# Performance work log

Measured on AMD Instinct MI355X. Metric: run time of the kernel, lower is better.

## Reference

```python
import jax, jax.numpy as jnp
import numpy as np

# ---- config (CSA layer, layer_idx=0 of pattern 'CSA,HCA') ----
B, T, C = 2, 2048, 2048
NH, NKV = 16, 8
HD = C // NH            # 128 head dim
ROPE_DIM = HD // 2      # partial RoPE dims (rope_head_dim=0 default)
RATIO = 4               # csa_compress_ratio
G = T // RATIO          # compressed groups (T divisible by ratio -> no pad)
IDX_NH = NH
IDX_HD = max(8, C // NH // 2)  # 64
TOPK = 64               # index_topk
Q_RANK = C // 2         # _default_rank
O_RPG = C // 2          # o_proj rank_per_group, o_groups=1


def rms_norm(x, eps=1e-6):
    return x * jax.lax.rsqrt(jnp.mean(jnp.square(x), axis=-1, keepdims=True) + eps)


def _rope(x, cos, sin):
    d = x.shape[-1] // 2
    x1, x2 = x[..., :d], x[..., d:]
    return jnp.concatenate([x1 * cos + x2 * sin, -x1 * sin + x2 * cos], axis=-1)


def partial_rope(x, cos, sin):
    # rotate only the last ROPE_DIM dims; cos/sin: [..., ROPE_DIM//2]
    xn, xr = x[..., :-ROPE_DIM], x[..., -ROPE_DIM:]
    return jnp.concatenate([xn, _rope(xr, cos, sin)], axis=-1)


def setup_inputs() -> dict:
    key = jax.random.key(0)
    ks = jax.random.split(key, 16)
    s = 0.02
    x = jax.random.normal(ks[0], (B, T, C), jnp.float32)
    pos = jnp.arange(T, dtype=jnp.float32)
    inv = 10000.0 ** (-jnp.arange(0, HD // 2, dtype=jnp.float32) / (HD // 2))
    ang = pos[:, None] * inv[None, :]  # [T, HD//2]
    p = lambda i, shp: jax.random.normal(ks[i], shp, jnp.float32) * s
    return dict(
        x=x, cos=jnp.cos(ang), sin=jnp.sin(ang),
        q_a_w=p(1, (C, Q_RANK)), q_b_w=p(2, (Q_RANK, NH * HD)),
        ck_w=p(3, (C, NKV * HD)), cv_w=p(4, (C, NKV * HD)), cg_w=p(5, (C, NKV * HD)),
        c_ape=p(6, (RATIO, NKV, HD)),
        iq_w=p(7, (C, IDX_NH * IDX_HD)), ik_w=p(8, (C, IDX_NH * IDX_HD)),
        ig_w=p(9, (C, IDX_NH * IDX_HD)), i_ape=p(10, (RATIO, IDX_NH, IDX_HD)),
        sink=jnp.zeros((NH,), jnp.float32),
        o_wa=p(11, (1, O_RPG, C)), o_pb=p(12, (O_RPG, C)),
    )


def reference(x, cos, sin, q_a_w, q_b_w, ck_w, cv_w, cg_w, c_ape,
              iq_w, ik_w, ig_w, i_ape, sink, o_wa, o_pb):
    NEG = jnp.finfo(jnp.float32).min
    half = ROPE_DIM // 2
    # --- low-rank queries + partial RoPE ---
    q = (x @ q_a_w @ q_b_w).reshape(B, T, NH, HD)
    q = partial_rope(q, cos[None, :, None, :half], sin[None, :, None, :half])
    # --- GatedCompressor: learned gated pooling over blocks of RATIO ---
    k = (x @ ck_w).reshape(B, G, RATIO, NKV, HD)
    v = (x @ cv_w).reshape(B, G, RATIO, NKV, HD)
    g = (x @ cg_w).reshape(B, G, RATIO, NKV, HD) + c_ape[None, None]
    w = jax.nn.softmax(g, axis=2)
    ck = (k * w).sum(2)  # [B,G,NKV,HD]
    cv = (v * w).sum(2)
    group_ends = jnp.arange(RATIO - 1, T, RATIO)  # [G]
    ckr = partial_rope(ck, cos[group_ends][None, :, None, :half],
                       sin[group_ends][None, :, None, :half])
    # --- LightningIndexer: compressed indexer keys + per-token top-k groups ---
    ik = (x @ ik_w).reshape(B, G, RATIO, IDX_NH, IDX_HD)
    ig = (x @ ig_w).reshape(B, G, RATIO, IDX_NH, IDX_HD) + i_ape[None, None]
    iw = jax.nn.softmax(ig, axis=2)
    ikeys = rms_norm((ik * iw).sum(2))  # [B,G,IH,IHD]
    iq = rms_norm((x @ iq_w).reshape(B, T, IDX_NH, IDX_HD))
    iscore = jnp.einsum('bthd,bghd->bhtg', iq, ikeys) * IDX_HD ** -0.5
    iscore = iscore.mean(axis=1)  # [B,T,G]
    causal = group_ends[None, None, :] <= jnp.arange(T)[None, :, None]
    iscore = jnp.where(causal, iscore, NEG)
    sel = jax.lax.top_k(iscore, TOPK)[1]  # [B,T,K]
    bidx = jnp.arange(B)[:, None, None]
    tidx = jnp.arange(T)[None, :, None]
    mask = jnp.zeros((B, T, G), bool).at[bidx, tidx, sel].set(True) & causal
    # --- compressed sparse attention with sink, GQA expand ---
    rep = NH // NKV
    kk = jnp.repeat(ckr, rep, axis=2)  # [B,G,NH,HD]
    vv = jnp.repeat(cv, rep, axis=2)
    scores = jnp.einsum('bthd,bghd->bhtg', q, kk) * HD ** -0.5
    scores = jnp.where(mask[:, None], scores, NEG)
    sinkb = jnp.broadcast_to(sink.reshape(1, NH, 1, 1), (B, NH, T, 1))
    probs = jax.nn.softmax(jnp.concatenate([scores, sinkb], axis=-1), axis=-1)[..., :-1]
    out = jnp.einsum('bhtg,bghd->bthd', probs, vv).reshape(B, T, C)
    # --- GroupedOutputProjection (o_groups=1) ---
    h = jnp.einsum('btgd,grd->btgr', out.reshape(B, T, 1, C), o_wa).reshape(B, T, -1)
    return rms_norm(h) @ o_pb
```

## Files before the change

### kernel.cpp

```cpp
#include <hip/hip_runtime.h>
#include <hip/hip_bf16.h>
#include <math.h>

constexpr int Bn  = 2;
constexpr int Tn  = 2048;
constexpr int NHn = 16;
constexpr int NKVn= 8;
constexpr int Gn  = 512;
constexpr int TKn = 64;

typedef __attribute__((ext_vector_type(8))) __bf16 bf16x8;
typedef __attribute__((ext_vector_type(4))) __bf16 bf16x4;
typedef __attribute__((ext_vector_type(2))) __bf16 bf16x2;
typedef __attribute__((ext_vector_type(4))) float f32x4;

__device__ __forceinline__ void gload_lds16(const void* g, void* l) {
  __builtin_amdgcn_global_load_lds(
      (const __attribute__((address_space(1))) unsigned int*)g,
      (__attribute__((address_space(3))) unsigned int*)l, 16, 0, 0);
}

__global__ __launch_bounds__(512) void gemm_kvqa_8ph(
    const __bf16* __restrict__ A, const __bf16* __restrict__ Bt,
    float* __restrict__ Cf, __bf16* __restrict__ Cq)
{
  constexpr int K = 2048;
  constexpr int NT = K / 64;
  __shared__ __bf16 lds[2][2][2][256][32];
  const int tid = threadIdx.x;
  const int wid = tid >> 6, lane = tid & 63;
  const int wm = wid >> 2, wn = wid & 3;
  const int row0 = blockIdx.y * 256, col0 = blockIdx.x * 256;

  f32x4 acc[8][4];
  const f32x4 zero = {0.f, 0.f, 0.f, 0.f};
  #pragma unroll
  for (int i = 0; i < 8; ++i)
    #pragma unroll
    for (int j = 0; j < 4; ++j) acc[i][j] = zero;

  auto stage1 = [&](int kt, int op, int ph, int buf) {
    long k0 = (long)kt * 64 + ph * 32;
    const __bf16* src = op ? Bt : A;
    const int base0 = op ? col0 : row0;
    #pragma unroll
    for (int l = 0; l < 2; ++l) {
      int u = l * 512 + tid;
      int r = u >> 2, c4 = u & 3;
      long csrc = (long)((c4 ^ ((r >> 1) & 3)) * 8);
      gload_lds16(src + (long)(base0 + r) * K + k0 + csrc, &lds[buf][op][ph][r][c4 * 8]);
    }
  };

  stage1(0, 0, 0, 0);
  stage1(0, 1, 0, 0);
  stage1(0, 0, 1, 0);
  stage1(0, 1, 1, 0);
  asm volatile("s_waitcnt vmcnt(4)" ::: "memory");
  asm volatile("s_barrier" ::: "memory");

  for (int kt = 0; kt < NT; ++kt) {
    const int buf = kt & 1;
    const bool pre = (kt + 1 < NT);
    bf16x8 afA[4], afB[4], bf[4];

    #pragma unroll
    for (int i = 0; i < 4; ++i) {
      int r = wm * 128 + i * 16 + (lane & 15);
      int c4 = (lane >> 4) ^ ((r >> 1) & 3);
      afA[i] = *(const bf16x8*)&lds[buf][0][0][r][c4 * 8];
    }
    #pragma unroll
    for (int i = 0; i < 4; ++i) {
      int r = wn * 64 + i * 16 + (lane & 15);
      int c4 = (lane >> 4) ^ ((r >> 1) & 3);
      bf[i] = *(const bf16x8*)&lds[buf][1][0][r][c4 * 8];
    }
    if (pre) stage1(kt + 1, 0, 0, buf ^ 1);
    asm volatile("s_barrier" ::: "memory");
    asm volatile("s_waitcnt lgkmcnt(0)" ::: "memory");
    __builtin_amdgcn_sched_barrier(0);
    __builtin_amdgcn_s_setprio(1);
    #pragma unroll
    for (int i = 0; i < 4; ++i)
      #pragma unroll
      for (int j = 0; j < 4; ++j)
        acc[i][j] = __builtin_amdgcn_mfma_f32_16x16x32_bf16(afA[i], bf[j], acc[i][j], 0, 0, 0);
    __builtin_amdgcn_s_setprio(0);
    asm volatile("s_barrier" ::: "memory");

    #pragma unroll
    for (int i = 0; i < 4; ++i) {
      int r = wm * 128 + (i + 4) * 16 + (lane & 15);
      int c4 = (lane >> 4) ^ ((r >> 1) & 3);
      afB[i] = *(const bf16x8*)&lds[buf][0][0][r][c4 * 8];
    }
    if (pre) {
      stage1(kt + 1, 1, 0, buf ^ 1);
      asm volatile("s_waitcnt vmcnt(4)" ::: "memory");
    } else {
      asm volatile("s_waitcnt vmcnt(0)" ::: "memory");
    }
    asm volatile("s_barrier" ::: "memory");
    asm volatile("s_waitcnt lgkmcnt(0)" ::: "memory");
    __builtin_amdgcn_sched_barrier(0);
    __builtin_amdgcn_s_setprio(1);
    #pragma unroll
    for (int i = 0; i < 4; ++i)
      #pragma unroll
      for (int j = 0; j < 4; ++j)
        acc[i + 4][j] = __builtin_amdgcn_mfma_f32_16x16x32_bf16(afB[i], bf[j], acc[i + 4][j], 0, 0, 0);
    __builtin_amdgcn_s_setprio(0);
    asm volatile("s_barrier" ::: "memory");

    #pragma unroll
    for (int i = 0; i < 4; ++i) {
      int r = wm * 128 + i * 16 + (lane & 15);
      int c4 = (lane >> 4) ^ ((r >> 1) & 3);
      afA[i] = *(const bf16x8*)&lds[buf][0][1][r][c4 * 8];
    }
    #pragma unroll
    for (int i = 0; i < 4; ++i) {
      int r = wn * 64 + i * 16 + (lane & 15);
      int c4 = (lane >> 4) ^ ((r >> 1) & 3);
      bf[i] = *(const bf16x8*)&lds[buf][1][1][r][c4 * 8];
    }
    if (pre) stage1(kt + 1, 0, 1, buf ^ 1);
    asm volatile("s_barrier" ::: "memory");
    asm volatile("s_waitcnt lgkmcnt(0)" ::: "memory");
    __builtin_amdgcn_sched_barrier(0);
    __builtin_amdgcn_s_setprio(1);
    #pragma unroll
    for (int i = 0; i < 4; ++i)
      #pragma unroll
      for (int j = 0; j < 4; ++j)
        acc[i][j] = __builtin_amdgcn_mfma_f32_16x16x32_bf16(afA[i], bf[j], acc[i][j], 0, 0, 0);
    __builtin_amdgcn_s_setprio(0);
    asm volatile("s_barrier" ::: "memory");

    #pragma unroll
    for (int i = 0; i < 4; ++i) {
      int r = wm * 128 + (i + 4) * 16 + (lane & 15);
      int c4 = (lane >> 4) ^ ((r >> 1) & 3);
      afB[i] = *(const bf16x8*)&lds[buf][0][1][r][c4 * 8];
    }
    if (pre) {
      stage1(kt + 1, 1, 1, buf ^ 1);
      asm volatile("s_waitcnt vmcnt(4)" ::: "memory");
    }
    asm volatile("s_barrier" ::: "memory");
    asm volatile("s_waitcnt lgkmcnt(0)" ::: "memory");
    __builtin_amdgcn_sched_barrier(0);
    __builtin_amdgcn_s_setprio(1);
    #pragma unroll
    for (int i = 0; i < 4; ++i)
      #pragma unroll
      for (int j = 0; j < 4; ++j)
        acc[i + 4][j] = __builtin_amdgcn_mfma_f32_16x16x32_bf16(afB[i], bf[j], acc[i + 4][j], 0, 0, 0);
    __builtin_amdgcn_s_setprio(0);
    asm volatile("s_barrier" ::: "memory");
  }

  const int crow = (lane >> 4) * 4, ccol = lane & 15;
  const bool isQ = (col0 >= 3072);
  #pragma unroll
  for (int mf = 0; mf < 8; ++mf)
    #pragma unroll
    for (int nf = 0; nf < 4; ++nf)
      #pragma unroll
      for (int j = 0; j < 4; ++j) {
        long r = row0 + wm * 128 + mf * 16 + crow + j;
        long c = col0 + wn * 64 + nf * 16 + ccol;
        float v = acc[mf][nf][j];
        if (isQ) Cq[r * 1024 + (c - 3072)] = (__bf16)v;
        else     Cf[r * 3072 + c] = v;
      }
}

template<int EPI>
__global__ __launch_bounds__(256) void gemm_pipe(
    const __bf16* __restrict__ A, const __bf16* __restrict__ Bt,
    void* __restrict__ Cp, int N, int K,
    const float* __restrict__ cosb, const float* __restrict__ sinb,
    const float* __restrict__ rs)
{
  const int NT = K >> 6;
  __shared__ __bf16 lds[2][2][2][128][32];
  const int tid = threadIdx.x;
  const int wid = tid >> 6, lane = tid & 63;
  const int wm = wid >> 1, wn = wid & 1;
  const int row0 = blockIdx.y * 128, col0 = blockIdx.x * 128;

  f32x4 acc[4][4];
  const f32x4 zero = {0.f, 0.f, 0.f, 0.f};
  #pragma unroll
  for (int i = 0; i < 4; ++i)
    #pragma unroll
    for (int j = 0; j < 4; ++j) acc[i][j] = zero;

  auto stage = [&](int kt, int p, int buf) {
    long k0 = (long)kt * 64 + p * 32;
    #pragma unroll
    for (int l = 0; l < 2; ++l) {
      int u = l * 256 + tid;
      int r = u >> 2, c4 = u & 3;
      long csrc = (long)((c4 ^ ((r >> 1) & 3)) * 8);
      gload_lds16(A  + (long)(row0 + r) * K + k0 + csrc, &lds[buf][0][p][r][c4 * 8]);
      gload_lds16(Bt + (long)(col0 + r) * K + k0 + csrc, &lds[buf][1][p][r][c4 * 8]);
    }
  };

  stage(0, 0, 0);
  stage(0, 1, 0);

  for (int kt = 0; kt < NT; ++kt) {
    const int buf = kt & 1;
    #pragma unroll
    for (int ph = 0; ph < 2; ++ph) {
      if (kt + 1 < NT) {
        stage(kt + 1, ph, buf ^ 1);
        asm volatile("s_waitcnt vmcnt(8)" ::: "memory");
      } else {
        if (ph == 0) asm volatile("s_waitcnt vmcnt(4)" ::: "memory");
        else         asm volatile("s_waitcnt vmcnt(0)" ::: "memory");
      }
      asm volatile("s_barrier" ::: "memory");
      bf16x8 af[4], bfr[4];
      #pragma unroll
      for (int mf = 0; mf < 4; ++mf) {
        int r = wm * 64 + mf * 16 + (lane & 15);
        int c4 = (lane >> 4) ^ ((r >> 1) & 3);
        af[mf] = *(const bf16x8*)&lds[buf][0][ph][r][c4 * 8];
      }
      #pragma unroll
      for (int nf = 0; nf < 4; ++nf) {
        int r = wn * 64 + nf * 16 + (lane & 15);
        int c4 = (lane >> 4) ^ ((r >> 1) & 3);
        bfr[nf] = *(const bf16x8*)&lds[buf][1][ph][r][c4 * 8];
      }
      __builtin_amdgcn_s_setprio(1);
      #pragma unroll
      for (int mf = 0; mf < 4; ++mf)
        #pragma unroll
        for (int nf = 0; nf < 4; ++nf)
          acc[mf][nf] = __builtin_amdgcn_mfma_f32_16x16x32_bf16(af[mf], bfr[nf], acc[mf][nf], 0, 0, 0);
      __builtin_amdgcn_s_setprio(0);
      asm volatile("s_barrier" ::: "memory");
    }
  }

  const int crow = (lane >> 4) * 4, ccol = lane & 15;
  if constexpr (EPI == 1) {
    __bf16* C = (__bf16*)Cp;
    if (wn == 1) {
      #pragma unroll
      for (int mf = 0; mf < 4; ++mf)
        #pragma unroll
        for (int j = 0; j < 4; ++j) {
          long r = row0 + wm * 64 + mf * 16 + crow + j;
          int t = (int)(r & 2047);
          #pragma unroll
          for (int nfp = 0; nfp < 2; ++nfp) {
            int jj = nfp * 16 + ccol;
            float c = cosb[t * 64 + jj], s = sinb[t * 64 + jj];
            float x1 = acc[mf][nfp][j];
            float x2 = acc[mf][nfp + 2][j];
            C[r * N + col0 + 64 + jj] = (__bf16)(x1 * c + x2 * s);
            C[r * N + col0 + 96 + jj] = (__bf16)(-x1 * s + x2 * c);
          }
        }
    } else {
      #pragma unroll
      for (int mf = 0; mf < 4; ++mf)
        #pragma unroll
        for (int nf = 0; nf < 4; ++nf)
          #pragma unroll
          for (int j = 0; j < 4; ++j) {
            long r = row0 + wm * 64 + mf * 16 + crow + j;
            long c = col0 + nf * 16 + ccol;
            C[r * N + c] = (__bf16)acc[mf][nf][j];
          }
    }
  } else {
    #pragma unroll
    for (int mf = 0; mf < 4; ++mf)
      #pragma unroll
      for (int nf = 0; nf < 4; ++nf)
        #pragma unroll
        for (int j = 0; j < 4; ++j) {
          long r = row0 + wm * 64 + mf * 16 + crow + j;
          long c = col0 + wn * 64 + nf * 16 + ccol;
          float v = acc[mf][nf][j];
          if constexpr (EPI == 2)
            ((float*)Cp)[r * N + c] = v * rs[r];
          else
            ((__bf16*)Cp)[r * N + c] = (__bf16)v;
        }
  }
}

__global__ __launch_bounds__(256) void gemm_split(
    const __bf16* __restrict__ Ah, const __bf16* __restrict__ Al,
    const __bf16* __restrict__ Bh, const __bf16* __restrict__ Bl,
    float* __restrict__ C, int M, int N, int K, float alpha,
    long sA, long sB, long sC)
{
  const int NT = K >> 5;
  __shared__ __bf16 lds[2][4][128][32];
  const int tid = threadIdx.x;
  const int wid = tid >> 6, lane = tid & 63;
  const int wm = wid >> 1, wn = wid & 1;
  const int row0 = blockIdx.y * 128, col0 = blockIdx.x * 128;
  Ah += (long)blockIdx.z * sA;  Al += (long)blockIdx.z * sA;
  Bh += (long)blockIdx.z * sB;  Bl += (long)blockIdx.z * sB;

  f32x4 acc[4][4];
  const f32x4 zero = {0.f, 0.f, 0.f, 0.f};
  #pragma unroll
  for (int i = 0; i < 4; ++i)
    #pragma unroll
    for (int j = 0; j < 4; ++j) acc[i][j] = zero;

  auto stage = [&](int kt, int buf) {
    long k0 = (long)kt * 32;
    #pragma unroll
    for (int l = 0; l < 2; ++l) {
      int u = l * 256 + tid;
      int r = u >> 2, c4 = u & 3;
      long csrc = (long)((c4 ^ ((r >> 1) & 3)) * 8);
      long ga = (long)(row0 + r) * K + k0 + csrc;
      long gb = (long)(col0 + r) * K + k0 + csrc;
      gload_lds16(Ah + ga, &lds[buf][0][r][c4 * 8]);
      gload_lds16(Al + ga, &lds[buf][1][r][c4 * 8]);
      gload_lds16(Bh + gb, &lds[buf][2][r][c4 * 8]);
      gload_lds16(Bl + gb, &lds[buf][3][r][c4 * 8]);
    }
  };

  stage(0, 0);

  for (int kt = 0; kt < NT; ++kt) {
    const int buf = kt & 1;
    if (kt + 1 < NT) {
      stage(kt + 1, buf ^ 1);
      asm volatile("s_waitcnt vmcnt(8)" ::: "memory");
    } else {
      asm volatile("s_waitcnt vmcnt(0)" ::: "memory");
    }
    asm volatile("s_barrier" ::: "memory");
    bf16x8 ah[4], al[4], bh[4], bl[4];
    #pragma unroll
    for (int mf = 0; mf < 4; ++mf) {
      int r = wm * 64 + mf * 16 + (lane & 15);
      int c4 = (lane >> 4) ^ ((r >> 1) & 3);
      ah[mf] = *(const bf16x8*)&lds[buf][0][r][c4 * 8];
      al[mf] = *(const bf16x8*)&lds[buf][1][r][c4 * 8];
    }
    #pragma unroll
    for (int nf = 0; nf < 4; ++nf) {
      int r = wn * 64 + nf * 16 + (lane & 15);
      int c4 = (lane >> 4) ^ ((r >> 1) & 3);
      bh[nf] = *(const bf16x8*)&lds[buf][2][r][c4 * 8];
      bl[nf] = *(const bf16x8*)&lds[buf][3][r][c4 * 8];
    }
    __builtin_amdgcn_s_setprio(1);
    #pragma unroll
    for (int mf = 0; mf < 4; ++mf)
      #pragma unroll
      for (int nf = 0; nf < 4; ++nf) {
        acc[mf][nf] = __builtin_amdgcn_mfma_f32_16x16x32_bf16(ah[mf], bh[nf], acc[mf][nf], 0, 0, 0);
        acc[mf][nf] = __builtin_amdgcn_mfma_f32_16x16x32_bf16(ah[mf], bl[nf], acc[mf][nf], 0, 0, 0);
        acc[mf][nf] = __builtin_amdgcn_mfma_f32_16x16x32_bf16(al[mf], bh[nf], acc[mf][nf], 0, 0, 0);
      }
    __builtin_amdgcn_s_setprio(0);
    asm volatile("s_barrier" ::: "memory");
  }

  const int crow = (lane >> 4) * 4, ccol = lane & 15;
  #pragma unroll
  for (int mf = 0; mf < 4; ++mf)
    #pragma unroll
    for (int nf = 0; nf < 4; ++nf)
      #pragma unroll
      for (int j = 0; j < 4; ++j) {
        long r = row0 + wm * 64 + mf * 16 + crow + j;
        long c = col0 + wn * 64 + nf * 16 + ccol;
        C[(long)blockIdx.z * sC + r * N + c] = acc[mf][nf][j] * alpha;
      }
}

__global__ __launch_bounds__(256) void prep_index(
    const float* __restrict__ x,
    const float* __restrict__ s0, const float* __restrict__ s1,
    const float* __restrict__ s2,
    __bf16* __restrict__ hiB, __bf16* __restrict__ loB, long dstride,
    __bf16* __restrict__ xhi, __bf16* __restrict__ xlo)
{
  __shared__ float tile[64][65];
  int z = blockIdx.y;
  int tid = threadIdx.x;
  if (z < 3) {
    const int R = 2048, Cc = 1024;
    const float* in = (z == 0) ? s0 : (z == 1) ? s1 : s2;
    __bf16* hiT = hiB + (long)z * dstride;
    __bf16* loT = loB + (long)z * dstride;
    int f = blockIdx.x;
    int r0 = (f >> 4) * 64, c0 = (f & 15) * 64;
    #pragma unroll
    for (int j = 0; j < 16; ++j) {
      int idx = tid + j * 256;
      int r = idx >> 6, c = idx & 63;
      tile[r][c] = in[(long)(r0 + r) * Cc + c0 + c];
    }
    __syncthreads();
    #pragma unroll
    for (int j = 0; j < 16; ++j) {
      int idx = tid + j * 256;
      int c = idx >> 6, r = idx & 63;
      float v = tile[r][c];
      __bf16 h = (__bf16)v;
      hiT[(long)(c0 + c) * R + r0 + r] = h;
      loT[(long)(c0 + c) * R + r0 + r] = (__bf16)(v - (float)h);
    }
  } else {
    for (long i = ((long)blockIdx.x * 256 + tid) * 4; i < 8388608; i += 524288) {
      float4 v = *(const float4*)&x[i];
      bf16x4 h, l;
      h[0] = (__bf16)v.x; l[0] = (__bf16)(v.x - (float)h[0]);
      h[1] = (__bf16)v.y; l[1] = (__bf16)(v.y - (float)h[1]);
      h[2] = (__bf16)v.z; l[2] = (__bf16)(v.z - (float)h[2]);
      h[3] = (__bf16)v.w; l[3] = (__bf16)(v.w - (float)h[3]);
      *(bf16x4*)&xhi[i] = h;
      *(bf16x4*)&xlo[i] = l;
    }
  }
}

__global__ __launch_bounds__(256) void prep_main(
    const float* __restrict__ s0, const float* __restrict__ s1,
    const float* __restrict__ s2, const float* __restrict__ s3,
    const float* __restrict__ s4, const float* __restrict__ s5,
    const float* __restrict__ wa,
    __bf16* __restrict__ W, long W2, __bf16* __restrict__ owab)
{
  __shared__ float tile[64][65];
  int z = blockIdx.y;
  int tid = threadIdx.x;
  if (z < 6) {
    int R, Cc, r0, c0;
    const float* in;
    if (z < 4) {
      R = 2048; Cc = 1024;
      in = (z == 0) ? s0 : (z == 1) ? s1 : (z == 2) ? s2 : s3;
      r0 = (blockIdx.x >> 4) * 64; c0 = (blockIdx.x & 15) * 64;
    } else {
      R = 1024; Cc = 2048;
      in = (z == 4) ? s4 : s5;
      r0 = (blockIdx.x >> 5) * 64; c0 = (blockIdx.x & 31) * 64;
    }
    __bf16* out = W + (long)z * W2;
    #pragma unroll
    for (int j = 0; j < 16; ++j) {
      int idx = tid + j * 256;
      int r = idx >> 6, c = idx & 63;
      tile[r][c] = in[(long)(r0 + r) * Cc + c0 + c];
    }
    __syncthreads();
    #pragma unroll
    for (int j = 0; j < 16; ++j) {
      int idx = tid + j * 256;
      int c = idx >> 6, r = idx & 63;
      out[(long)(c0 + c) * R + r0 + r] = (__bf16)tile[r][c];
    }
  } else {
    for (long i = ((long)blockIdx.x * 256 + tid) * 4; i < 2097152; i += 524288) {
      float4 v = *(const float4*)&wa[i];
      bf16x4 o;
      o[0] = (__bf16)v.x; o[1] = (__bf16)v.y; o[2] = (__bf16)v.z; o[3] = (__bf16)v.w;
      *(bf16x4*)&owab[i] = o;
    }
  }
}

__global__ __launch_bounds__(256) void reduce_ckcv(
    const float* __restrict__ base, const float* __restrict__ c_ape,
    const float* __restrict__ cosb, const float* __restrict__ sinb,
    __bf16* __restrict__ ckb, __bf16* __restrict__ cvb)
{
  __shared__ float sck[256];
  const long S = 3072;
  int tid = threadIdx.x;
  int c = blockIdx.x * 256 + tid;
  int g = blockIdx.y, b = blockIdx.z;
  long row0 = (long)b * Tn + 4 * g;
  float lg[4], mx = -1e30f;
  #pragma unroll
  for (int r = 0; r < 4; ++r) {
    lg[r] = base[(row0 + r) * S + 2048 + c] + c_ape[r * 1024 + c];
    mx = fmaxf(mx, lg[r]);
  }
  float ssum = 0.f;
  #pragma unroll
  for (int r = 0; r < 4; ++r) { lg[r] = expf(lg[r] - mx); ssum += lg[r]; }
  float inv = 1.f / ssum, ak = 0.f, av = 0.f;
  #pragma unroll
  for (int r = 0; r < 4; ++r) {
    float w = lg[r] * inv;
    ak = fmaf(base[(row0 + r) * S + c],        w, ak);
    av = fmaf(base[(row0 + r) * S + 1024 + c], w, av);
  }
  long o = ((long)b * Gn + g) * 1024 + c;
  cvb[o] = (__bf16)av;
  sck[tid] = ak;
  __syncthreads();
  int d = c & 127;
  float outk = ak;
  if (d >= 64) {
    int t = 4 * g + 3;
    if (d < 96) {
      int j = d - 64;
      outk = ak * cosb[t * 64 + j] + sck[tid + 32] * sinb[t * 64 + j];
    } else {
      int j = d - 96;
      outk = -sck[tid - 32] * sinb[t * 64 + j] + ak * cosb[t * 64 + j];
    }
  }
  ckb[o] = (__bf16)outk;
}

__global__ __launch_bounds__(1024) void reduce_idx_fused(
    const float* __restrict__ base, const float* __restrict__ i_ape,
    __bf16* __restrict__ khi, __bf16* __restrict__ klo,
    __bf16* __restrict__ qhi, __bf16* __restrict__ qlo)
{
  const long S = 3072;
  int tid = threadIdx.x;
  int bid = blockIdx.x;
  if (bid < Gn * Bn) {
    int g = bid & (Gn - 1), b = bid >> 9;
    long row0 = (long)b * Tn + 4 * g;
    float lg[4], mx = -1e30f;
    #pragma unroll
    for (int r = 0; r < 4; ++r) {
      lg[r] = base[(row0 + r) * S + 1024 + tid] + i_ape[r * 1024 + tid];
      mx = fmaxf(mx, lg[r]);
    }
    float ssum = 0.f;
    #pragma unroll
    for (int r = 0; r < 4; ++r) { lg[r] = expf(lg[r] - mx); ssum += lg[r]; }
    float inv = 1.f / ssum, red = 0.f;
    #pragma unroll
    for (int r = 0; r < 4; ++r) red = fmaf(base[(row0 + r) * S + tid], lg[r] * inv, red);
    float ss = red * red;
    #pragma unroll
    for (int o = 32; o; o >>= 1) ss += __shfl_xor(ss, o);
    float v = red * rsqrtf(ss * (1.f / 64.f) + 1e-6f);
    long oi = ((long)b * Gn + g) * 1024 + tid;
    __bf16 h = (__bf16)v;
    khi[oi] = h; klo[oi] = (__bf16)(v - (float)h);
  } else {
    long row = bid - Gn * Bn;
    float v = base[row * S + 2048 + tid];
    float ss = v * v;
    #pragma unroll
    for (int o = 32; o; o >>= 1) ss += __shfl_xor(ss, o);
    float y = v * rsqrtf(ss * (1.f / 64.f) + 1e-6f);
    __bf16 h = (__bf16)y;
    qhi[row * 1024 + tid] = h;
    qlo[row * 1024 + tid] = (__bf16)(y - (float)h);
  }
}

__global__ __launch_bounds__(256) void rms_scales(
    const __bf16* __restrict__ h, float* __restrict__ rs)
{
  int wid = threadIdx.x >> 6, lane = threadIdx.x & 63;
  long row = (long)blockIdx.x * 4 + wid;
  const __bf16* hr = h + row * 1024 + lane * 16;
  bf16x8 a = *(const bf16x8*)hr;
  bf16x8 b = *(const bf16x8*)(hr + 8);
  float ss = 0.f;
  #pragma unroll
  for (int j = 0; j < 8; ++j) {
    float x = (float)a[j], y = (float)b[j];
    ss = fmaf(x, x, ss); ss = fmaf(y, y, ss);
  }
  #pragma unroll
  for (int o = 1; o < 64; o <<= 1) ss += __shfl_xor(ss, o);
  if (lane == 0) rs[row] = rsqrtf(ss * (1.f / 1024.f) + 1e-6f);
}

__global__ __launch_bounds__(256) void topk_kernel(
    const float* __restrict__ iscore, int* __restrict__ selidx, int* __restrict__ selcnt)
{
  int wave = threadIdx.x >> 6, lane = threadIdx.x & 63;
  long bt = (long)blockIdx.x * 4 + wave;
  int t = (int)(bt % Tn);
  const float* row = iscore + bt * Gn;
  int ng = (t + 1) >> 2; if (ng > Gn) ng = Gn;
  int cap = ng < TKn ? ng : TKn;
  float s[8];
  #pragma unroll
  for (int j = 0; j < 8; ++j) {
    int g = lane + 64 * j;
    s[j] = (g < ng) ? row[g] : -INFINITY;
  }
  int* outp = selidx + bt * TKn;
  for (int it = 0; it < cap; ++it) {
    float bv = -INFINITY; int bi = Gn;
    #pragma unroll
    for (int j = 0; j < 8; ++j) {
      int g = lane + 64 * j;
      if (s[j] > bv) { bv = s[j]; bi = g; }
    }
    #pragma unroll
    for (int o = 1; o < 64; o <<= 1) {
      float ov = __shfl_xor(bv, o); int oi = __shfl_xor(bi, o);
      if (ov > bv || (ov == bv && oi < bi)) { bv = ov; bi = oi; }
    }
    if (lane == 0) outp[it] = bi;
    #pragma unroll
    for (int j = 0; j < 8; ++j) if (bi == lane + 64 * j) s[j] = -INFINITY;
  }
  for (int it = cap + lane; it < TKn; it += 64) outp[it] = 0;
  if (lane == 0) selcnt[bt] = cap;
}

__global__ __launch_bounds__(256) void attn_kernel(
    const __bf16* __restrict__ q, const __bf16* __restrict__ ckb,
    const __bf16* __restrict__ cvb, const int* __restrict__ selidx,
    const int* __restrict__ selcnt, const float* __restrict__ sink,
    __bf16* __restrict__ out)
{
  __shared__ float sS[4][16][68];
  __shared__ int   sG[4][64];
  const float scale = 0.08838834764831845f;
  int wid = threadIdx.x >> 6, lane = threadIdx.x & 63;
  long bt = (long)blockIdx.x * 4 + wid;
  int b = (int)(bt >> 11);
  int cnt = selcnt[bt];
  int gid = (lane < cnt) ? selidx[bt * TKn + lane] : 0;
  sG[wid][lane] = gid;

  int grp = lane >> 3;
  int sub = lane & 7;
  int h0 = grp * 2, h1 = h0 + 1;
  int d0 = sub * 16;

  const __bf16* qrow = q + bt * 2048;
  float q0[16], q1[16];
  {
    bf16x8 a0 = *(const bf16x8*)&qrow[h0 * 128 + d0];
    bf16x8 a1 = *(const bf16x8*)&qrow[h0 * 128 + d0 + 8];
    bf16x8 c0 = *(const bf16x8*)&qrow[h1 * 128 + d0];
    bf16x8 c1 = *(const bf16x8*)&qrow[h1 * 128 + d0 + 8];
    #pragma unroll
    for (int j = 0; j < 8; ++j) {
      q0[j] = (float)a0[j]; q0[8 + j] = (float)a1[j];
      q1[j] = (float)c0[j]; q1[8 + j] = (float)c1[j];
    }
  }
  __syncthreads();

  for (int i0 = 0; i0 < 64; i0 += 8) {
    #pragma unroll
    for (int u = 0; u < 8; ++u) {
      int i = i0 + u;
      int g = sG[wid][i];
      const __bf16* kr = ckb + ((long)(b * Gn + g)) * 1024 + lane * 16;
      bf16x8 k0 = *(const bf16x8*)kr;
      bf16x8 k1 = *(const bf16x8*)(kr + 8);
      float p0 = 0.f, p1 = 0.f;
      #pragma unroll
      for (int j = 0; j < 8; ++j) {
        float kv = (float)k0[j];
        p0 = fmaf(kv, q0[j], p0); p1 = fmaf(kv, q1[j], p1);
      }
      #pragma unroll
      for (int j = 0; j < 8; ++j) {
        float kv = (float)k1[j];
        p0 = fmaf(kv, q0[8 + j], p0); p1 = fmaf(kv, q1[8 + j], p1);
      }
      p0 += __shfl_xor(p0, 1); p0 += __shfl_xor(p0, 2); p0 += __shfl_xor(p0, 4);
      p1 += __shfl_xor(p1, 1); p1 += __shfl_xor(p1, 2); p1 += __shfl_xor(p1, 4);
      if (sub == 0) { sS[wid][h0][i] = p0; sS[wid][h1][i] = p1; }
    }
  }
  __syncthreads();

  {
    int h = lane >> 2, qtr = lane & 3;
    float sv[16];
    float mx = -INFINITY;
    #pragma unroll
    for (int j = 0; j < 16; ++j) {
      int i = qtr * 16 + j;
      float s = (i < cnt) ? sS[wid][h][i] * scale : -INFINITY;
      sv[j] = s; mx = fmaxf(mx, s);
    }
    mx = fmaxf(mx, __shfl_xor(mx, 1));
    mx = fmaxf(mx, __shfl_xor(mx, 2));
    float snk = sink[h];
    mx = fmaxf(mx, snk);
    float sum = 0.f;
    #pragma unroll
    for (int j = 0; j < 16; ++j) { sv[j] = __expf(sv[j] - mx); sum += sv[j]; }
    sum += __shfl_xor(sum, 1);
    sum += __shfl_xor(sum, 2);
    sum += __expf(snk - mx);
    float inv = 1.f / sum;
    #pragma unroll
    for (int j = 0; j < 16; ++j) sS[wid][h][qtr * 16 + j] = sv[j] * inv;
  }
  __syncthreads();

  float o0[16], o1[16];
  #pragma unroll
  for (int j = 0; j < 16; ++j) { o0[j] = 0.f; o1[j] = 0.f; }
  for (int i0 = 0; i0 < 64; i0 += 8) {
    #pragma unroll
    for (int u = 0; u < 8; ++u) {
      int i = i0 + u;
      int g = sG[wid][i];
      float p0 = sS[wid][h0][i], p1 = sS[wid][h1][i];
      const __bf16* vr = cvb + ((long)(b * Gn + g)) * 1024 + lane * 16;
      bf16x8 v0 = *(const bf16x8*)vr;
      bf16x8 v1 = *(const bf16x8*)(vr + 8);
      #pragma unroll
      for (int j = 0; j < 8; ++j) {
        float vv = (float)v0[j];
        o0[j] = fmaf(p0, vv, o0[j]); o1[j] = fmaf(p1, vv, o1[j]);
      }
      #pragma unroll
      for (int j = 0; j < 8; ++j) {
        float vv = (float)v1[j];
        o0[8 + j] = fmaf(p0, vv, o0[8 + j]); o1[8 + j] = fmaf(p1, vv, o1[8 + j]);
      }
    }
  }
  __bf16* ob = out + bt * 2048;
  bf16x8 w;
  #pragma unroll
  for (int j = 0; j < 8; ++j) w[j] = (__bf16)o0[j];
  *(bf16x8*)&ob[h0 * 128 + d0] = w;
  #pragma unroll
  for (int j = 0; j < 8; ++j) w[j] = (__bf16)o0[8 + j];
  *(bf16x8*)&ob[h0 * 128 + d0 + 8] = w;
  #pragma unroll
  for (int j = 0; j < 8; ++j) w[j] = (__bf16)o1[j];
  *(bf16x8*)&ob[h1 * 128 + d0] = w;
  #pragma unroll
  for (int j = 0; j < 8; ++j) w[j] = (__bf16)o1[8 + j];
  *(bf16x8*)&ob[h1 * 128 + d0 + 8] = w;
}

extern "C" void kernel_launch(void* const* d_in, const int* in_sizes, int n_in,
                              void* d_out, int out_size, void* d_ws, size_t ws_size,
                              hipStream_t stream) {
  const float* x     = (const float*)d_in[0];
  const float* cosb  = (const float*)d_in[1];
  const float* sinb  = (const float*)d_in[2];
  const float* q_a_w = (const float*)d_in[3];
  const float* q_b_w = (const float*)d_in[4];
  const float* ck_w  = (const float*)d_in[5];
  const float* cv_w  = (const float*)d_in[6];
  const float* cg_w  = (const float*)d_in[7];
  const float* c_ape = (const float*)d_in[8];
  const float* iq_w  = (const float*)d_in[9];
  const float* ik_w  = (const float*)d_in[10];
  const float* ig_w  = (const float*)d_in[11];
  const float* i_ape = (const float*)d_in[12];
  const float* sink  = (const float*)d_in[13];
  const float* o_wa  = (const float*)d_in[14];
  const float* o_pb  = (const float*)d_in[15];
  float* outp = (float*)d_out;
  float* ws = (float*)d_ws;

  const long F  = 4194304;
  const long M1 = 1048576;

  float* b_all = ws;
  float*  iscore = ws + F;
  __bf16* oatt_b = (__bf16*)(ws + F);
  __bf16* hb_b   = (__bf16*)ws;

  __bf16* iq_hi = (__bf16*)d_out;
  __bf16* iq_lo = (__bf16*)d_out + 4194304;
  __bf16* qb    = (__bf16*)d_out;

  char* tp = (char*)(ws + 3 * F);
  __bf16* ckb = (__bf16*)tp;     tp += (size_t)M1 * 4;
  __bf16* cvb = (__bf16*)tp;     tp += (size_t)M1 * 4;
  int*   selidx = (int*)tp;      tp += 2097152;
  int*   selcnt = selidx + Bn * Tn * TKn;
  __bf16* ikeys_hi = (__bf16*)tp; tp += 2097152;
  __bf16* ikeys_lo = (__bf16*)tp; tp += 2097152;
  __bf16* xhi = (__bf16*)tp;      tp += 16777216;
  __bf16* xlo = (__bf16*)tp;      tp += 16777216;
  __bf16* W   = (__bf16*)tp;      tp += 7 * 4194304;
  __bf16* qa_buf = (__bf16*)tp;   tp += 8388608;
  float*  rs     = (float*)tp;    tp += 16384;
  const long W2 = 2097152;
  __bf16* Whi = W;            __bf16* Wlo = W + 3 * W2;
  __bf16* ckT  = W;
  __bf16* qbT  = W + 4*W2;
  __bf16* opbT = W + 5*W2;   __bf16* owab = W + 6*W2;

  prep_index<<<dim3(512, 4), 256, 0, stream>>>(
      x, ik_w, ig_w, iq_w, Whi, Wlo, W2, xhi, xlo);

  gemm_split<<<dim3(24, 32), 256, 0, stream>>>(xhi, xlo, Whi, Wlo, b_all,
      4096, 3072, 2048, 1.f, 0, 0, 0);
  reduce_idx_fused<<<dim3(Gn * Bn + Bn * Tn), 1024, 0, stream>>>(
      b_all, i_ape, ikeys_hi, ikeys_lo, iq_hi, iq_lo);

  gemm_split<<<dim3(4, 16, 2), 256, 0, stream>>>(iq_hi, iq_lo, ikeys_hi, ikeys_lo, iscore,
      2048, 512, 1024, 1.f / 128.f, (long)2048 * 1024, (long)512 * 1024, (long)2048 * 512);
  topk_kernel<<<dim3(Bn * Tn / 4), 256, 0, stream>>>(iscore, selidx, selcnt);

  prep_main<<<dim3(512, 7), 256, 0, stream>>>(
      ck_w, cv_w, cg_w, q_a_w, q_b_w, o_pb, o_wa, W, W2, owab);

  gemm_kvqa_8ph<<<dim3(16, 16), 512, 0, stream>>>(xhi, ckT, b_all, qa_buf);
  reduce_ckcv<<<dim3(4, Gn, Bn), 256, 0, stream>>>(b_all, c_ape, cosb, sinb, ckb, cvb);

  gemm_pipe<1><<<dim3(16, 32), 256, 0, stream>>>(
      qa_buf, qbT, qb, 2048, 1024, cosb, sinb, nullptr);

  attn_kernel<<<dim3(Bn * Tn / 4), 256, 0, stream>>>(qb, ckb, cvb, selidx, selcnt, sink, oatt_b);

  gemm_pipe<0><<<dim3(8, 32), 256, 0, stream>>>(
      oatt_b, owab, hb_b, 1024, 2048, nullptr, nullptr, nullptr);
  rms_scales<<<dim3(1024), 256, 0, stream>>>(hb_b, rs);
  gemm_pipe<2><<<dim3(16, 32), 256, 0, stream>>>(
      hb_b, opbT, outp, 2048, 1024, nullptr, nullptr, rs);
}
```

Measured before the change: 525.1 us.

## Add 8-phase pipelined split-bf16 GEMM for index projection

Adds a new 512-thread split-precision (hi/lo bf16) GEMM kernel using 256x192 tiles. Its K loop is broken into four phases, each interleaving LDS fragment reads, async global-to-LDS prefetch of the next tile, barriers and priority-raised MFMA bursts. It replaces the older 128-tile gemm_split for the large 4096x3072x2048 index projection. The aim is better overlap of memory traffic with the three-MFMA-per-product split arithmetic and better data reuse, at the cost of more registers and tighter hand-written vmcnt synchronisation.

```diff
diff --git a/kernel.cpp b/kernel.cpp
--- a/kernel.cpp
+++ b/kernel.cpp
@@ -174,6 +174,178 @@
         float v = acc[mf][nf][j];
         if (isQ) Cq[r * 1024 + (c - 3072)] = (__bf16)v;
         else     Cf[r * 3072 + c] = v;
+      }
+}
+
+__global__ __launch_bounds__(512) void gemm_split_8ph(
+    const __bf16* __restrict__ Ah, const __bf16* __restrict__ Al,
+    const __bf16* __restrict__ Bh, const __bf16* __restrict__ Bl,
+    float* __restrict__ C, int M, int N, int K, float alpha)
+{
+  const int NT = K >> 5;
+  constexpr int LA_H = 0;
+  constexpr int LA_L = 8192;
+  constexpr int LB_H = 16384;
+  constexpr int LBUF = 28672;
+  __shared__ __bf16 sm[2 * LBUF];
+  const int tid = threadIdx.x;
+  const int wid = tid >> 6, lane = tid & 63;
+  const int wm = wid >> 2, wn = wid & 3;
+  const int row0 = blockIdx.y * 256, col0 = blockIdx.x * 192;
+
+  f32x4 acc[8][3];
+  const f32x4 zero = {0.f, 0.f, 0.f, 0.f};
+  #pragma unroll
+  for (int i = 0; i < 8; ++i)
+    #pragma unroll
+    for (int j = 0; j < 3; ++j) acc[i][j] = zero;
+
+  auto stageA = [&](int kt, int buf, int which) {
+    long k0 = (long)kt * 32;
+    const __bf16* src = which ? Al : Ah;
+    __bf16* dst = &sm[buf * LBUF + (which ? LA_L : LA_H)];
+    #pragma unroll
+    for (int l = 0; l < 2; ++l) {
+      int u = l * 512 + tid;
+      int r = u >> 2, c4 = u & 3;
+      long csrc = (long)((c4 ^ ((r >> 1) & 3)) * 8);
+      gload_lds16(src + (long)(row0 + r) * K + k0 + csrc, dst + u * 8);
+    }
+  };
+  auto stageB = [&](int kt, int buf) {
+    long k0 = (long)kt * 32;
+    __bf16* dst = &sm[buf * LBUF + LB_H];
+    #pragma unroll
+    for (int l = 0; l < 3; ++l) {
+      int u = l * 512 + tid;
+      int v = (u < 768) ? u : u - 768;
+      const __bf16* src = (u < 768) ? Bh : Bl;
+      int r = v >> 2, c4 = v & 3;
+      long csrc = (long)((c4 ^ ((r >> 1) & 3)) * 8);
+      gload_lds16(src + (long)(col0 + r) * K + k0 + csrc, dst + u * 8);
+    }
+  };
+
+  stageB(0, 0);
+  stageA(0, 0, 0);
+  stageA(0, 0, 1);
+  asm volatile("s_waitcnt vmcnt(2)" ::: "memory");
+  asm volatile("s_barrier" ::: "memory");
+
+  for (int kt = 0; kt < NT; ++kt) {
+    const int buf = kt & 1;
+    const bool pre = (kt + 1 < NT);
+    bf16x8 a_h[4], a_l[4], b_h[3], b_l[3];
+
+    #pragma unroll
+    for (int i = 0; i < 4; ++i) {
+      int r = wm * 128 + i * 16 + (lane & 15);
+      int c4 = (lane >> 4) ^ ((r >> 1) & 3);
+      a_h[i] = *(const bf16x8*)&sm[buf * LBUF + LA_H + r * 32 + c4 * 8];
+    }
+    #pragma unroll
+    for (int j = 0; j < 3; ++j) {
+      int r = wn * 48 + j * 16 + (lane & 15);
+      int c4 = (lane >> 4) ^ ((r >> 1) & 3);
+      b_h[j] = *(const bf16x8*)&sm[buf * LBUF + LB_H + r * 32 + c4 * 8];
+    }
+    if (pre) {
+      stageB(kt + 1, buf ^ 1);
+      asm volatile("s_waitcnt vmcnt(3)" ::: "memory");
+    } else {
+      asm volatile("s_waitcnt vmcnt(0)" ::: "memory");
+    }
+    asm volatile("s_barrier" ::: "memory");
+    asm volatile("s_waitcnt lgkmcnt(0)" ::: "memory");
+    __builtin_amdgcn_sched_barrier(0);
+    __builtin_amdgcn_s_setprio(1);
+    #pragma unroll
+    for (int i = 0; i < 4; ++i)
+      #pragma unroll
+      for (int j = 0; j < 3; ++j)
+        acc[i][j] = __builtin_amdgcn_mfma_f32_16x16x32_bf16(a_h[i], b_h[j], acc[i][j], 0, 0, 0);
+    __builtin_amdgcn_s_setprio(0);
+    asm volatile("s_barrier" ::: "memory");
+
+    #pragma unroll
+    for (int i = 0; i < 4; ++i) {
+      int r = wm * 128 + i * 16 + (lane & 15);
+      int c4 = (lane >> 4) ^ ((r >> 1) & 3);
+      a_l[i] = *(const bf16x8*)&sm[buf * LBUF + LA_L + r * 32 + c4 * 8];
+    }
+    #pragma unroll
+    for (int j = 0; j < 3; ++j) {
+      int r = wn * 48 + j * 16 + (lane & 15);
+      int c4 = (lane >> 4) ^ ((r >> 1) & 3);
+      b_l[j] = *(const bf16x8*)&sm[buf * LBUF + LB_H + 6144 + r * 32 + c4 * 8];
+    }
+    if (pre) stageA(kt + 1, buf ^ 1, 0);
+    asm volatile("s_barrier" ::: "memory");
+    asm volatile("s_waitcnt lgkmcnt(0)" ::: "memory");
+    __builtin_amdgcn_sched_barrier(0);
+    __builtin_amdgcn_s_setprio(1);
+    #pragma unroll
+    for (int i = 0; i < 4; ++i)
+      #pragma unroll
+      for (int j = 0; j < 3; ++j) {
+        acc[i][j] = __builtin_amdgcn_mfma_f32_16x16x32_bf16(a_h[i], b_l[j], acc[i][j], 0, 0, 0);
+        acc[i][j] = __builtin_amdgcn_mfma_f32_16x16x32_bf16(a_l[i], b_h[j], acc[i][j], 0, 0, 0);
+      }
+    __builtin_amdgcn_s_setprio(0);
+    asm volatile("s_barrier" ::: "memory");
+
+    #pragma unroll
+    for (int i = 0; i < 4; ++i) {
+      int r = wm * 128 + (i + 4) * 16 + (lane & 15);
+      int c4 = (lane >> 4) ^ ((r >> 1) & 3);
+      a_h[i] = *(const bf16x8*)&sm[buf * LBUF + LA_H + r * 32 + c4 * 8];
+    }
+    if (pre) stageA(kt + 1, buf ^ 1, 1);
+    asm volatile("s_barrier" ::: "memory");
+    asm volatile("s_waitcnt lgkmcnt(0)" ::: "memory");
+    __builtin_amdgcn_sched_barrier(0);
+    __builtin_amdgcn_s_setprio(1);
+    #pragma unroll
+    for (int i = 0; i < 4; ++i)
+      #pragma unroll
+      for (int j = 0; j < 3; ++j)
+        acc[i + 4][j] = __builtin_amdgcn_mfma_f32_16x16x32_bf16(a_h[i], b_h[j], acc[i + 4][j], 0, 0, 0);
+    __builtin_amdgcn_s_setprio(0);
+    asm volatile("s_barrier" ::: "memory");
+
+    #pragma unroll
+    for (int i = 0; i < 4; ++i) {
+      int r = wm * 128 + (i + 4) * 16 + (lane & 15);
+      int c4 = (lane >> 4) ^ ((r >> 1) & 3);
+      a_l[i] = *(const bf16x8*)&sm[buf * LBUF + LA_L + r * 32 + c4 * 8];
+    }
+    if (pre)
+      asm volatile("s_waitcnt vmcnt(2)" ::: "memory");
+    asm volatile("s_barrier" ::: "memory");
+    asm volatile("s_waitcnt lgkmcnt(0)" ::: "memory");
+    __builtin_amdgcn_sched_barrier(0);
+    __builtin_amdgcn_s_setprio(1);
+    #pragma unroll
+    for (int i = 0; i < 4; ++i)
+      #pragma unroll
+      for (int j = 0; j < 3; ++j) {
+        acc[i + 4][j] = __builtin_amdgcn_mfma_f32_16x16x32_bf16(a_h[i], b_l[j], acc[i + 4][j], 0, 0, 0);
+        acc[i + 4][j] = __builtin_amdgcn_mfma_f32_16x16x32_bf16(a_l[i], b_h[j], acc[i + 4][j], 0, 0, 0);
+      }
+    __builtin_amdgcn_s_setprio(0);
+    asm volatile("s_barrier" ::: "memory");
+  }
+
+  const int crow = (lane >> 4) * 4, ccol = lane & 15;
+  #pragma unroll
+  for (int mf = 0; mf < 8; ++mf)
+    #pragma unroll
+    for (int nf = 0; nf < 3; ++nf)
+      #pragma unroll
+      for (int j = 0; j < 4; ++j) {
+        long r = row0 + wm * 128 + mf * 16 + crow + j;
+        long c = col0 + wn * 48 + nf * 16 + ccol;
+        C[r * N + c] = acc[mf][nf][j] * alpha;
       }
 }
 
@@ -809,8 +981,8 @@
   prep_index<<<dim3(512, 4), 256, 0, stream>>>(
       x, ik_w, ig_w, iq_w, Whi, Wlo, W2, xhi, xlo);
 
-  gemm_split<<<dim3(24, 32), 256, 0, stream>>>(xhi, xlo, Whi, Wlo, b_all,
-      4096, 3072, 2048, 1.f, 0, 0, 0);
+  gemm_split_8ph<<<dim3(16, 16), 512, 0, stream>>>(xhi, xlo, Whi, Wlo, b_all,
+      4096, 3072, 2048, 1.f);
   reduce_idx_fused<<<dim3(Gn * Bn + Bn * Tn), 1024, 0, stream>>>(
       b_all, i_ape, ikeys_hi, ikeys_lo, iq_hi, iq_lo);
 
```

Result: faster. 500.5 us (-4.7%).
